# Optimization experiments

Measured on AMD Instinct MI355X. Metric: run time of the kernel, lower is better.

## Reference

```python
import jax, jax.numpy as jnp
import numpy as np

N, E = 50000, 800000
IN_DIM, HID, OUT = 64, 128, 64
EPS = 1e-5  # BatchNorm eps


def setup_inputs() -> dict:
    key = jax.random.key(0)
    ks = jax.random.split(key, 16)
    def w(k, i, o):
        return jax.random.normal(k, (i, o), jnp.float32) / np.float32(np.sqrt(i))
    def bn(k):
        km, kv = jax.random.split(k)
        return (jnp.ones((HID,), jnp.float32),                       # gamma
                jnp.zeros((HID,), jnp.float32),                      # beta
                0.1 * jax.random.normal(km, (HID,), jnp.float32),    # running mean
                0.5 + jax.random.uniform(kv, (HID,), jnp.float32))   # running var
    g0, be0, m0, v0 = bn(ks[6])
    g1, be1, m1, v1 = bn(ks[7])
    g2, be2, m2, v2 = bn(ks[8])
    return {
        "x":   jax.random.normal(ks[0], (N, IN_DIM), jnp.float32),
        "src": jax.random.randint(ks[1], (E,), 0, N, jnp.int32),
        "dst": jax.random.randint(ks[2], (E,), 0, N, jnp.int32),
        "W0": w(ks[3], IN_DIM, HID), "b0": jnp.zeros((HID,), jnp.float32),
        "g0": g0, "be0": be0, "m0": m0, "v0": v0,
        "W1": w(ks[4], HID, HID), "b1": jnp.zeros((HID,), jnp.float32),
        "g1": g1, "be1": be1, "m1": m1, "v1": v1,
        "W2": w(ks[5], HID, HID), "b2": jnp.zeros((HID,), jnp.float32),
        "g2": g2, "be2": be2, "m2": m2, "v2": v2,
        "Wm1": w(ks[9], HID, HID), "bm1": jnp.zeros((HID,), jnp.float32),
        "Wm2": w(ks[10], HID, OUT), "bm2": jnp.zeros((OUT,), jnp.float32),
    }


def gcn_conv(x, src, dst, W, b):
    # PyG GCNConv: h = x @ W; add self loops; symmetric normalization; scatter-add; + bias
    h = x @ W                                                     # [N, F]
    ones = jnp.ones((src.shape[0],), h.dtype)
    deg = 1.0 + jax.ops.segment_sum(ones, dst, num_segments=N)   # self loop adds 1
    dinv = jax.lax.rsqrt(deg)                                     # deg^-1/2 (deg >= 1)
    coef = (dinv[src] * dinv[dst])[:, None]                       # per-edge norm
    agg = jax.ops.segment_sum(h[src] * coef, dst, num_segments=N)
    return agg + h * (dinv * dinv)[:, None] + b                   # self-loop term + bias


def bn_relu(x, g, be, m, v):
    # eval-mode BatchNorm1d followed by ReLU (dropout is identity in eval)
    return jax.nn.relu((x - m) * jax.lax.rsqrt(v + EPS) * g + be)


def reference(x, src, dst,
              W0, b0, g0, be0, m0, v0,
              W1, b1, g1, be1, m1, v1,
              W2, b2, g2, be2, m2, v2,
              Wm1, bm1, Wm2, bm2):
    h = bn_relu(gcn_conv(x, src, dst, W0, b0), g0, be0, m0, v0)
    h = bn_relu(gcn_conv(h, src, dst, W1, b1), g1, be1, m1, v1)
    h = bn_relu(gcn_conv(h, src, dst, W2, b2), g2, be2, m2, v2)
    h = jax.nn.relu(h @ Wm1 + bm1)
    return h @ Wm2 + bm2
```

## Files before the change

### kernel.cpp

```cpp
#include <hip/hip_runtime.h>
#include <hip/hip_fp16.h>

#define BN_EPS 1e-5f
#define BK 512
#define NBMAX 128
#define ECH 8192
#define BCAP 9216

typedef _Float16 half_t;
typedef _Float16 half8 __attribute__((ext_vector_type(8)));
typedef float floatx4 __attribute__((ext_vector_type(4)));


__global__ __launch_bounds__(256) void scatter_cvt_kernel(
    const int* __restrict__ src, const int* __restrict__ dst,
    int* __restrict__ bcursor, int2* __restrict__ tmp,
    const float* __restrict__ x, __half* __restrict__ x16,
    int E, int nb, int sb, int n4) {
  const int t = threadIdx.x;
  if (blockIdx.x >= sb) {
    int i = (blockIdx.x - sb) * 256 + t;
    if (i < n4) {
      float4 v = *(const float4*)(x + (size_t)i * 4);
      union { __half h[4]; float2 f; } u;
      u.h[0] = __float2half_rn(v.x);
      u.h[1] = __float2half_rn(v.y);
      u.h[2] = __float2half_rn(v.z);
      u.h[3] = __float2half_rn(v.w);
      *(float2*)(x16 + (size_t)i * 4) = u.f;
    }
    return;
  }
  __shared__ int h[NBMAX];
  for (int i = t; i < nb; i += 256) h[i] = 0;
  __syncthreads();
  const int base = blockIdx.x * ECH;
#pragma unroll 8
  for (int p = 0; p < ECH / 256; ++p) {
    int e = base + p * 256 + t;
    if (e < E) atomicAdd(&h[dst[e] >> 9], 1);
  }
  __syncthreads();
  for (int i = t; i < nb; i += 256) {
    int c = h[i];
    h[i] = c ? (i * BCAP + atomicAdd(&bcursor[i], c)) : 0;
  }
  __syncthreads();
#pragma unroll 8
  for (int p = 0; p < ECH / 256; ++p) {
    int e = base + p * 256 + t;
    if (e < E) {
      int s = src[e], d = dst[e];
      int pos = atomicAdd(&h[d >> 9], 1);
      tmp[pos] = make_int2(s, d);
    }
  }
}

__global__ __launch_bounds__(256) void bucket_finalize_kernel(
    const int2* __restrict__ tmp, const int* __restrict__ bcursor,
    int* __restrict__ offs, int* __restrict__ offe, float* __restrict__ dinv,
    int* __restrict__ esrc, __half* __restrict__ x16, int n) {
  __shared__ int deg[BK];
  __shared__ int cur[BK];
  __shared__ float fdi[BK];
  __shared__ int ts[256];
  const int t = threadIdx.x;
  const int b = blockIdx.x;
  const int nbase = b * BK;
  const int nn = min(BK, n - nbase);
  const int cnt = bcursor[b];
  const int2* tp = tmp + (size_t)b * BCAP;
  for (int i = t; i < nn; i += 256) deg[i] = 0;
  __syncthreads();
  for (int e = t; e < cnt; e += 256)
    atomicAdd(&deg[tp[e].y - nbase], 1);
  __syncthreads();
  int d0 = (2 * t < nn) ? deg[2 * t] : 0;
  int d1 = (2 * t + 1 < nn) ? deg[2 * t + 1] : 0;
  ts[t] = d0 + d1;
  __syncthreads();
  for (int o = 1; o < 256; o <<= 1) {
    int v = (t >= o) ? ts[t - o] : 0;
    __syncthreads();
    ts[t] += v;
    __syncthreads();
  }
  int base = b * BCAP + ((t == 0) ? 0 : ts[t - 1]);
  if (2 * t < nn) {
    float di = rsqrtf(1.0f + (float)d0);
    offs[nbase + 2 * t] = base;
    offe[nbase + 2 * t] = base + d0;
    cur[2 * t] = base;
    fdi[2 * t] = di;
    dinv[nbase + 2 * t] = di;
  }
  if (2 * t + 1 < nn) {
    float di = rsqrtf(1.0f + (float)d1);
    offs[nbase + 2 * t + 1] = base + d0;
    offe[nbase + 2 * t + 1] = base + d0 + d1;
    cur[2 * t + 1] = base + d0;
    fdi[2 * t + 1] = di;
    dinv[nbase + 2 * t + 1] = di;
  }
  __syncthreads();
  for (int e = t; e < cnt; e += 256) {
    int2 r = tp[e];
    int pos = atomicAdd(&cur[r.y - nbase], 1);
    esrc[pos] = r.x;
  }
  __half2* xp = (__half2*)x16;
  for (int i = t; i < nn * 32; i += 256) {
    int nl = i >> 5;
    size_t idx = (((size_t)(nbase + nl)) << 5) + (i & 31);
    float2 v = __half22float2(xp[idx]);
    float s = fdi[nl];
    xp[idx] = __floats2half2_rn(v.x * s, v.y * s);
  }
}


template <int FIN, int FOUT, int EPI, bool HALFOUT>
__global__ __launch_bounds__(256) void mgemm_kernel(
    const __half* __restrict__ X, const float* __restrict__ W,
    const float* __restrict__ bias, const float* __restrict__ gam,
    const float* __restrict__ bet, const float* __restrict__ mean,
    const float* __restrict__ var, void* __restrict__ Yv, int n) {
  constexpr int LDK = 72;
  constexpr int NCI = FOUT / 16;
  __shared__ half_t Asm[128 * LDK];
  __shared__ half_t Bsm[FOUT * LDK];

  const int t = threadIdx.x;
  const int wave = t >> 6, lane = t & 63;
  const int quad = lane >> 4, l16 = lane & 15;
  const int rowBase = blockIdx.x * 128;

  floatx4 acc[2][NCI];
#pragma unroll
  for (int i = 0; i < 2; ++i)
#pragma unroll
    for (int ci = 0; ci < NCI; ++ci) acc[i][ci] = (floatx4){0.f, 0.f, 0.f, 0.f};

  for (int kc = 0; kc < FIN; kc += 64) {
    __syncthreads();
    {
      const int kq = t & 15, m0 = t >> 4;
#pragma unroll
      for (int p = 0; p < 8; ++p) {
        int m = p * 16 + m0;
        int row = rowBase + m;
        uint2 v = make_uint2(0u, 0u);
        if (row < n) v = *(const uint2*)(X + (size_t)row * FIN + kc + kq * 4);
        *(uint2*)&Asm[m * LDK + kq * 4] = v;
      }
    }
    {
#pragma unroll
      for (int c0 = 0; c0 < FOUT * 16; c0 += 256) {
        int c = c0 + t;
        int nn = c % FOUT;
        int kg = (c / FOUT) * 4;
        const float* wp = W + (size_t)(kc + kg) * FOUT + nn;
        half_t* d = &Bsm[nn * LDK + kg];
        d[0] = (half_t)wp[0];
        d[1] = (half_t)wp[FOUT];
        d[2] = (half_t)wp[2 * FOUT];
        d[3] = (half_t)wp[3 * FOUT];
      }
    }
    __syncthreads();
#pragma unroll
    for (int kk = 0; kk < 2; ++kk) {
      half8 a0 = *(const half8*)&Asm[(wave * 32 + l16) * LDK + kk * 32 + quad * 8];
      half8 a1 = *(const half8*)&Asm[(wave * 32 + 16 + l16) * LDK + kk * 32 + quad * 8];
#pragma unroll
      for (int ci = 0; ci < NCI; ++ci) {
        half8 b = *(const half8*)&Bsm[(ci * 16 + l16) * LDK + kk * 32 + quad * 8];
        acc[0][ci] = __builtin_amdgcn_mfma_f32_16x16x32_f16(a0, b, acc[0][ci], 0, 0, 0);
        acc[1][ci] = __builtin_amdgcn_mfma_f32_16x16x32_f16(a1, b, acc[1][ci], 0, 0, 0);
      }
    }
  }

  float sc[NCI], sh[NCI];
#pragma unroll
  for (int ci = 0; ci < NCI; ++ci) {
    int col = ci * 16 + l16;
    if constexpr (EPI == 3) {
      float s = gam[col] * rsqrtf(var[col] + BN_EPS);
      sc[ci] = s;
      sh[ci] = (bias[col] - mean[col]) * s + bet[col];
    } else if constexpr (EPI == 1 || EPI == 2) {
      sc[ci] = 1.f;
      sh[ci] = bias[col];
    } else {
      sc[ci] = 1.f;
      sh[ci] = 0.f;
    }
  }
  float rs[2][4];
  if constexpr (EPI == 4) {
#pragma unroll
    for (int ri = 0; ri < 2; ++ri)
#pragma unroll
      for (int r = 0; r < 4; ++r) {
        int row = rowBase + wave * 32 + ri * 16 + quad * 4 + r;
        rs[ri][r] = (row < n) ? bias[row] : 0.f;
      }
  }
#pragma unroll
  for (int ri = 0; ri < 2; ++ri)
#pragma unroll
    for (int ci = 0; ci < NCI; ++ci) {
      int col = ci * 16 + l16;
#pragma unroll
      for (int r = 0; r < 4; ++r) {
        int row = rowBase + wave * 32 + ri * 16 + quad * 4 + r;
        if (row < n) {
          float v = acc[ri][ci][r];
          if constexpr (EPI == 4) v *= rs[ri][r];
          if constexpr (EPI == 1 || EPI == 2 || EPI == 3) v = fmaf(v, sc[ci], sh[ci]);
          if constexpr (EPI == 1 || EPI == 3) v = fmaxf(v, 0.f);
          if constexpr (HALFOUT)
            ((half_t*)Yv)[(size_t)row * FOUT + col] = (half_t)v;
          else
            ((float*)Yv)[(size_t)row * FOUT + col] = v;
        }
      }
    }
}


__global__ __launch_bounds__(256) void mlp_kernel(
    const __half* __restrict__ X, const float* __restrict__ W1,
    const float* __restrict__ b1f, const float* __restrict__ W2,
    const float* __restrict__ b2f, float* __restrict__ Y, int n) {
  constexpr int LDK = 72;
  constexpr int LDK2 = 136;
  __shared__ half_t smem[(128 + 64) * LDK2];
  half_t* As1 = smem;
  half_t* Bs1 = smem + 128 * LDK;
  half_t* As2 = smem;
  half_t* Bs2 = smem + 128 * LDK2;

  const int t = threadIdx.x;
  const int wave = t >> 6, lane = t & 63;
  const int quad = lane >> 4, l16 = lane & 15;
  const int rowBase = blockIdx.x * 128;

  floatx4 acc[2][8];
#pragma unroll
  for (int i = 0; i < 2; ++i)
#pragma unroll
    for (int ci = 0; ci < 8; ++ci) acc[i][ci] = (floatx4){0.f, 0.f, 0.f, 0.f};

  for (int kc = 0; kc < 128; kc += 64) {
    __syncthreads();
    {
      const int kq = t & 15, m0 = t >> 4;
#pragma unroll
      for (int p = 0; p < 8; ++p) {
        int m = p * 16 + m0;
        int row = rowBase + m;
        uint2 v = make_uint2(0u, 0u);
        if (row < n) v = *(const uint2*)(X + (size_t)row * 128 + kc + kq * 4);
        *(uint2*)&As1[m * LDK + kq * 4] = v;
      }
    }
    {
#pragma unroll
      for (int c0 = 0; c0 < 128 * 16; c0 += 256) {
        int c = c0 + t;
        int nn = c & 127;
        int kg = (c >> 7) << 2;
        const float* wp = W1 + (size_t)(kc + kg) * 128 + nn;
        half_t* d = &Bs1[nn * LDK + kg];
        d[0] = (half_t)wp[0];
        d[1] = (half_t)wp[128];
        d[2] = (half_t)wp[256];
        d[3] = (half_t)wp[384];
      }
    }
    __syncthreads();
#pragma unroll
    for (int kk = 0; kk < 2; ++kk) {
      half8 a0 = *(const half8*)&As1[(wave * 32 + l16) * LDK + kk * 32 + quad * 8];
      half8 a1 = *(const half8*)&As1[(wave * 32 + 16 + l16) * LDK + kk * 32 + quad * 8];
#pragma unroll
      for (int ci = 0; ci < 8; ++ci) {
        half8 b = *(const half8*)&Bs1[(ci * 16 + l16) * LDK + kk * 32 + quad * 8];
        acc[0][ci] = __builtin_amdgcn_mfma_f32_16x16x32_f16(a0, b, acc[0][ci], 0, 0, 0);
        acc[1][ci] = __builtin_amdgcn_mfma_f32_16x16x32_f16(a1, b, acc[1][ci], 0, 0, 0);
      }
    }
  }
  __syncthreads();

#pragma unroll
  for (int ri = 0; ri < 2; ++ri)
#pragma unroll
    for (int ci = 0; ci < 8; ++ci) {
      int col = ci * 16 + l16;
      float bz = b1f[col];
#pragma unroll
      for (int r = 0; r < 4; ++r) {
        int m = wave * 32 + ri * 16 + quad * 4 + r;
        As2[m * LDK2 + col] = (half_t)fmaxf(acc[ri][ci][r] + bz, 0.f);
      }
    }
  {
#pragma unroll
    for (int c0 = 0; c0 < 64 * 32; c0 += 256) {
      int c = c0 + t;
      int nn = c & 63;
      int kg = (c >> 6) << 2;
      const float* wp = W2 + (size_t)kg * 64 + nn;
      half_t* d = &Bs2[nn * LDK2 + kg];
      d[0] = (half_t)wp[0];
      d[1] = (half_t)wp[64];
      d[2] = (half_t)wp[128];
      d[3] = (half_t)wp[192];
    }
  }
  __syncthreads();

  floatx4 acc2[2][4];
#pragma unroll
  for (int i = 0; i < 2; ++i)
#pragma unroll
    for (int ci = 0; ci < 4; ++ci) acc2[i][ci] = (floatx4){0.f, 0.f, 0.f, 0.f};
#pragma unroll
  for (int kk = 0; kk < 4; ++kk) {
    half8 a0 = *(const half8*)&As2[(wave * 32 + l16) * LDK2 + kk * 32 + quad * 8];
    half8 a1 = *(const half8*)&As2[(wave * 32 + 16 + l16) * LDK2 + kk * 32 + quad * 8];
#pragma unroll
    for (int ci = 0; ci < 4; ++ci) {
      half8 b = *(const half8*)&Bs2[(ci * 16 + l16) * LDK2 + kk * 32 + quad * 8];
      acc2[0][ci] = __builtin_amdgcn_mfma_f32_16x16x32_f16(a0, b, acc2[0][ci], 0, 0, 0);
      acc2[1][ci] = __builtin_amdgcn_mfma_f32_16x16x32_f16(a1, b, acc2[1][ci], 0, 0, 0);
    }
  }
#pragma unroll
  for (int ri = 0; ri < 2; ++ri)
#pragma unroll
    for (int ci = 0; ci < 4; ++ci) {
      int col = ci * 16 + l16;
      float bz = b2f[col];
#pragma unroll
      for (int r = 0; r < 4; ++r) {
        int row = rowBase + wave * 32 + ri * 16 + quad * 4 + r;
        if (row < n) Y[(size_t)row * 64 + col] = acc2[ri][ci][r] + bz;
      }
    }
}


__global__ __launch_bounds__(256) void agg64_kernel(
    const __half* __restrict__ h, const int* __restrict__ offs,
    const int* __restrict__ offe, const int* __restrict__ esrc,
    const float* __restrict__ dinv, __half* __restrict__ out, int n) {
  int gi = blockIdx.x * 4 + (threadIdx.x >> 6);
  if (gi >= n) return;
  const int lane = threadIdx.x & 63;
  const float di = dinv[gi];

  float a0 = 0.f, a1 = 0.f, a2 = 0.f, a3 = 0.f;
  int e = offs[gi];
  const int e1 = offe[gi];
  const int m = e1 - 1;
  for (; e < e1; e += 4) {
    int s0 = esrc[e];
    int s1 = esrc[min(e + 1, m)];
    int s2 = esrc[min(e + 2, m)];
    int s3 = esrc[min(e + 3, m)];
    float h0 = __half2float(h[((size_t)s0 << 6) + lane]);
    float h1 = __half2float(h[((size_t)s1 << 6) + lane]);
    float h2 = __half2float(h[((size_t)s2 << 6) + lane]);
    float h3 = __half2float(h[((size_t)s3 << 6) + lane]);
    if (e + 1 >= e1) h1 = 0.f;
    if (e + 2 >= e1) h2 = 0.f;
    if (e + 3 >= e1) h3 = 0.f;
    a0 += h0; a1 += h1; a2 += h2; a3 += h3;
  }
  float a = (a0 + a1) + (a2 + a3);
  a += __half2float(h[((size_t)gi << 6) + lane]);
  out[((size_t)gi << 6) + lane] = __float2half_rn(di * a);
}

__global__ __launch_bounds__(256) void agg128_bn_kernel(
    const __half* __restrict__ h, const int* __restrict__ offs,
    const int* __restrict__ offe, const int* __restrict__ esrc,
    const float* __restrict__ dinv,
    const float* __restrict__ bias, const float* __restrict__ gam,
    const float* __restrict__ bet, const float* __restrict__ mean,
    const float* __restrict__ var, __half* __restrict__ out, int n) {
  int gi = blockIdx.x * 4 + (threadIdx.x >> 6);
  if (gi >= n) return;
  const int lane = threadIdx.x & 63;
  const int c = lane << 1;
  const __half2* hp = (const __half2*)h;
  const float di = dinv[gi];

  float ax = 0.f, ay = 0.f, bx = 0.f, by = 0.f;
  float cx = 0.f, cy = 0.f, dx = 0.f, dy = 0.f;
  int e = offs[gi];
  const int e1 = offe[gi];
  const int m = e1 - 1;
  for (; e < e1; e += 4) {
    int s0 = esrc[e];
    int s1 = esrc[min(e + 1, m)];
    int s2 = esrc[min(e + 2, m)];
    int s3 = esrc[min(e + 3, m)];
    float2 h0 = __half22float2(hp[((size_t)s0 << 6) + lane]);
    float2 h1 = __half22float2(hp[((size_t)s1 << 6) + lane]);
    float2 h2 = __half22float2(hp[((size_t)s2 << 6) + lane]);
    float2 h3 = __half22float2(hp[((size_t)s3 << 6) + lane]);
    if (e + 1 >= e1) { h1.x = 0.f; h1.y = 0.f; }
    if (e + 2 >= e1) { h2.x = 0.f; h2.y = 0.f; }
    if (e + 3 >= e1) { h3.x = 0.f; h3.y = 0.f; }
    ax += h0.x; ay += h0.y; bx += h1.x; by += h1.y;
    cx += h2.x; cy += h2.y; dx += h3.x; dy += h3.y;
  }
  ax = (ax + bx) + (cx + dx);
  ay = (ay + by) + (cy + dy);
  float2 hs = __half22float2(hp[((size_t)gi << 6) + lane]);
  ax = di * (ax + hs.x);
  ay = di * (ay + hs.y);

  float2 bv = *(const float2*)(bias + c);
  float2 gv = *(const float2*)(gam + c);
  float2 bev = *(const float2*)(bet + c);
  float2 mv = *(const float2*)(mean + c);
  float2 vv = *(const float2*)(var + c);
  float s0 = gv.x * rsqrtf(vv.x + BN_EPS);
  float s1 = gv.y * rsqrtf(vv.y + BN_EPS);
  float o0 = fmaxf(fmaf(ax + bv.x - mv.x, s0, bev.x), 0.f);
  float o1 = fmaxf(fmaf(ay + bv.y - mv.y, s1, bev.y), 0.f);
  ((__half2*)out)[((size_t)gi << 6) + lane] = __floats2half2_rn(o0, o1);
}


static inline size_t alignup(size_t x, size_t a) { return (x + a - 1) & ~(a - 1); }

extern "C" void kernel_launch(void* const* d_in, const int* in_sizes, int n_in,
                              void* d_out, int out_size, void* d_ws, size_t ws_size,
                              hipStream_t stream) {
  const float* x   = (const float*)d_in[0];
  const int*   src = (const int*)d_in[1];
  const int*   dst = (const int*)d_in[2];
  const float* W0  = (const float*)d_in[3];
  const float* b0  = (const float*)d_in[4];
  const float* g0  = (const float*)d_in[5];
  const float* be0 = (const float*)d_in[6];
  const float* m0  = (const float*)d_in[7];
  const float* v0  = (const float*)d_in[8];
  const float* W1  = (const float*)d_in[9];
  const float* b1  = (const float*)d_in[10];
  const float* g1  = (const float*)d_in[11];
  const float* be1 = (const float*)d_in[12];
  const float* m1  = (const float*)d_in[13];
  const float* v1  = (const float*)d_in[14];
  const float* W2  = (const float*)d_in[15];
  const float* b2  = (const float*)d_in[16];
  const float* g2  = (const float*)d_in[17];
  const float* be2 = (const float*)d_in[18];
  const float* m2  = (const float*)d_in[19];
  const float* v2  = (const float*)d_in[20];
  const float* Wm1 = (const float*)d_in[21];
  const float* bm1 = (const float*)d_in[22];
  const float* Wm2 = (const float*)d_in[23];
  const float* bm2 = (const float*)d_in[24];

  const int N = in_sizes[0] / 64;
  const int E = in_sizes[1];

  char* p = (char*)d_ws;
  auto take = [&](size_t bytes) {
    char* r = p;
    p += alignup(bytes, 256);
    return r;
  };
  const int nbk = (N + BK - 1) / BK;
  int*    bcursor= (int*)take(NBMAX * 4);
  int*    offs   = (int*)take((size_t)N * 4);
  int*    offe   = (int*)take((size_t)N * 4);
  float*  dinv   = (float*)take((size_t)N * 4);
  int*    esrc   = (int*)take((size_t)nbk * BCAP * 4);
  int2*   tmp    = (int2*)take((size_t)nbk * BCAP * 8);
  __half* x16    = (__half*)take((size_t)N * 64 * 2);
  __half* aggx16 = (__half*)take((size_t)N * 64 * 2);
  __half* t0     = (__half*)take((size_t)N * 128 * 2);
  __half* t1     = (__half*)take((size_t)N * 128 * 2);
  float*  yout   = (float*)d_out;

  const int TB = 256;
  const int sb = (E + ECH - 1) / ECH;
  const int n4 = N * 16;
  const int cb = (n4 + 255) / 256;

  hipMemsetAsync(bcursor, 0, NBMAX * 4, stream);
  scatter_cvt_kernel<<<sb + cb, TB, 0, stream>>>(src, dst, bcursor, tmp,
                                                 x, x16, E, nbk, sb, n4);
  bucket_finalize_kernel<<<nbk, TB, 0, stream>>>(tmp, bcursor, offs, offe,
                                                 dinv, esrc, x16, N);

  const int gemmGrid = (N + 127) / 128;
  const int aggGrid = (N + 3) / 4;

  agg64_kernel<<<aggGrid, TB, 0, stream>>>(x16, offs, offe, esrc, dinv, aggx16, N);
  mgemm_kernel<64, 128, 3, true><<<gemmGrid, TB, 0, stream>>>(
      aggx16, W0, b0, g0, be0, m0, v0, t0, N);
  mgemm_kernel<128, 128, 4, true><<<gemmGrid, TB, 0, stream>>>(
      t0, W1, dinv, nullptr, nullptr, nullptr, nullptr, t1, N);
  agg128_bn_kernel<<<aggGrid, TB, 0, stream>>>(t1, offs, offe, esrc, dinv,
                                               b1, g1, be1, m1, v1, t0, N);
  mgemm_kernel<128, 128, 4, true><<<gemmGrid, TB, 0, stream>>>(
      t0, W2, dinv, nullptr, nullptr, nullptr, nullptr, t1, N);
  agg128_bn_kernel<<<aggGrid, TB, 0, stream>>>(t1, offs, offe, esrc, dinv,
                                               b2, g2, be2, m2, v2, t0, N);
  mlp_kernel<<<gemmGrid, TB, 0, stream>>>(t0, Wm1, bm1, Wm2, bm2, yout, N);
}
```

Baseline: 336.7 us.

## Split wave across edges with 8-byte row loads and shuffle reduction in aggregation

New measurement: 332.1 us. About the same (-1.4%).

```diff
diff --git a/kernel.cpp b/kernel.cpp
--- a/kernel.cpp
+++ b/kernel.cpp
@@ -363,29 +363,48 @@
   int gi = blockIdx.x * 4 + (threadIdx.x >> 6);
   if (gi >= n) return;
   const int lane = threadIdx.x & 63;
+  const int q = lane >> 4;
+  const int j = lane & 15;
+  const __half2* hp = (const __half2*)h;
   const float di = dinv[gi];
 
-  float a0 = 0.f, a1 = 0.f, a2 = 0.f, a3 = 0.f;
+  float ax = 0.f, ay = 0.f, az = 0.f, aw = 0.f;
+  float bx = 0.f, by = 0.f, bz = 0.f, bw = 0.f;
   int e = offs[gi];
   const int e1 = offe[gi];
   const int m = e1 - 1;
-  for (; e < e1; e += 4) {
-    int s0 = esrc[e];
-    int s1 = esrc[min(e + 1, m)];
-    int s2 = esrc[min(e + 2, m)];
-    int s3 = esrc[min(e + 3, m)];
-    float h0 = __half2float(h[((size_t)s0 << 6) + lane]);
-    float h1 = __half2float(h[((size_t)s1 << 6) + lane]);
-    float h2 = __half2float(h[((size_t)s2 << 6) + lane]);
-    float h3 = __half2float(h[((size_t)s3 << 6) + lane]);
-    if (e + 1 >= e1) h1 = 0.f;
-    if (e + 2 >= e1) h2 = 0.f;
-    if (e + 3 >= e1) h3 = 0.f;
-    a0 += h0; a1 += h1; a2 += h2; a3 += h3;
-  }
-  float a = (a0 + a1) + (a2 + a3);
-  a += __half2float(h[((size_t)gi << 6) + lane]);
-  out[((size_t)gi << 6) + lane] = __float2half_rn(di * a);
+  for (; e < e1; e += 8) {
+    int i0 = e + q;
+    int i1 = e + 4 + q;
+    int s0 = esrc[min(i0, m)];
+    int s1 = esrc[min(i1, m)];
+    uint2 r0 = *(const uint2*)(hp + (((size_t)s0) << 5) + j * 2);
+    uint2 r1 = *(const uint2*)(hp + (((size_t)s1) << 5) + j * 2);
+    if (i0 >= e1) { r0.x = 0u; r0.y = 0u; }
+    if (i1 >= e1) { r1.x = 0u; r1.y = 0u; }
+    float2 p0 = __half22float2(*(__half2*)&r0.x);
+    float2 p1 = __half22float2(*(__half2*)&r0.y);
+    float2 q0 = __half22float2(*(__half2*)&r1.x);
+    float2 q1 = __half22float2(*(__half2*)&r1.y);
+    ax += p0.x; ay += p0.y; az += p1.x; aw += p1.y;
+    bx += q0.x; by += q0.y; bz += q1.x; bw += q1.y;
+  }
+  ax += bx; ay += by; az += bz; aw += bw;
+  ax += __shfl_xor(ax, 16); ay += __shfl_xor(ay, 16);
+  az += __shfl_xor(az, 16); aw += __shfl_xor(aw, 16);
+  ax += __shfl_xor(ax, 32); ay += __shfl_xor(ay, 32);
+  az += __shfl_xor(az, 32); aw += __shfl_xor(aw, 32);
+  if (q == 0) {
+    uint2 rs = *(const uint2*)(hp + (((size_t)gi) << 5) + j * 2);
+    float2 s0 = __half22float2(*(__half2*)&rs.x);
+    float2 s1 = __half22float2(*(__half2*)&rs.y);
+    __half2 h0 = __floats2half2_rn(di * (ax + s0.x), di * (ay + s0.y));
+    __half2 h1 = __floats2half2_rn(di * (az + s1.x), di * (aw + s1.y));
+    uint2 ov;
+    ov.x = *(unsigned*)&h0;
+    ov.y = *(unsigned*)&h1;
+    *(uint2*)((__half2*)out + (((size_t)gi) << 5) + j * 2) = ov;
+  }
 }
 
 __global__ __launch_bounds__(256) void agg128_bn_kernel(
@@ -398,46 +417,60 @@
   int gi = blockIdx.x * 4 + (threadIdx.x >> 6);
   if (gi >= n) return;
   const int lane = threadIdx.x & 63;
-  const int c = lane << 1;
+  const int hh = lane >> 5;
+  const int j = lane & 31;
   const __half2* hp = (const __half2*)h;
   const float di = dinv[gi];
 
-  float ax = 0.f, ay = 0.f, bx = 0.f, by = 0.f;
-  float cx = 0.f, cy = 0.f, dx = 0.f, dy = 0.f;
+  float ax = 0.f, ay = 0.f, az = 0.f, aw = 0.f;
+  float bx = 0.f, by = 0.f, bz = 0.f, bw = 0.f;
   int e = offs[gi];
   const int e1 = offe[gi];
   const int m = e1 - 1;
   for (; e < e1; e += 4) {
-    int s0 = esrc[e];
-    int s1 = esrc[min(e + 1, m)];
-    int s2 = esrc[min(e + 2, m)];
-    int s3 = esrc[min(e + 3, m)];
-    float2 h0 = __half22float2(hp[((size_t)s0 << 6) + lane]);
-    float2 h1 = __half22float2(hp[((size_t)s1 << 6) + lane]);
-    float2 h2 = __half22float2(hp[((size_t)s2 << 6) + lane]);
-    float2 h3 = __half22float2(hp[((size_t)s3 << 6) + lane]);
-    if (e + 1 >= e1) { h1.x = 0.f; h1.y = 0.f; }
-    if (e + 2 >= e1) { h2.x = 0.f; h2.y = 0.f; }
-    if (e + 3 >= e1) { h3.x = 0.f; h3.y = 0.f; }
-    ax += h0.x; ay += h0.y; bx += h1.x; by += h1.y;
-    cx += h2.x; cy += h2.y; dx += h3.x; dy += h3.y;
-  }
-  ax = (ax + bx) + (cx + dx);
-  ay = (ay + by) + (cy + dy);
-  float2 hs = __half22float2(hp[((size_t)gi << 6) + lane]);
-  ax = di * (ax + hs.x);
-  ay = di * (ay + hs.y);
-
-  float2 bv = *(const float2*)(bias + c);
-  float2 gv = *(const float2*)(gam + c);
-  float2 bev = *(const float2*)(bet + c);
-  float2 mv = *(const float2*)(mean + c);
-  float2 vv = *(const float2*)(var + c);
-  float s0 = gv.x * rsqrtf(vv.x + BN_EPS);
-  float s1 = gv.y * rsqrtf(vv.y + BN_EPS);
-  float o0 = fmaxf(fmaf(ax + bv.x - mv.x, s0, bev.x), 0.f);
-  float o1 = fmaxf(fmaf(ay + bv.y - mv.y, s1, bev.y), 0.f);
-  ((__half2*)out)[((size_t)gi << 6) + lane] = __floats2half2_rn(o0, o1);
+    int i0 = e + hh;
+    int i1 = e + 2 + hh;
+    int s0 = esrc[min(i0, m)];
+    int s1 = esrc[min(i1, m)];
+    uint2 r0 = *(const uint2*)(hp + (((size_t)s0) << 6) + j * 2);
+    uint2 r1 = *(const uint2*)(hp + (((size_t)s1) << 6) + j * 2);
+    if (i0 >= e1) { r0.x = 0u; r0.y = 0u; }
+    if (i1 >= e1) { r1.x = 0u; r1.y = 0u; }
+    float2 p0 = __half22float2(*(__half2*)&r0.x);
+    float2 p1 = __half22float2(*(__half2*)&r0.y);
+    float2 q0 = __half22float2(*(__half2*)&r1.x);
+    float2 q1 = __half22float2(*(__half2*)&r1.y);
+    ax += p0.x; ay += p0.y; az += p1.x; aw += p1.y;
+    bx += q0.x; by += q0.y; bz += q1.x; bw += q1.y;
+  }
+  ax += bx; ay += by; az += bz; aw += bw;
+  ax += __shfl_xor(ax, 32); ay += __shfl_xor(ay, 32);
+  az += __shfl_xor(az, 32); aw += __shfl_xor(aw, 32);
+  if (hh == 0) {
+    uint2 rs = *(const uint2*)(hp + (((size_t)gi) << 6) + j * 2);
+    float2 s0 = __half22float2(*(__half2*)&rs.x);
+    float2 s1 = __half22float2(*(__half2*)&rs.y);
+    float v0 = di * (ax + s0.x);
+    float v1 = di * (ay + s0.y);
+    float v2 = di * (az + s1.x);
+    float v3 = di * (aw + s1.y);
+    const int c = j * 4;
+    float4 bv = *(const float4*)(bias + c);
+    float4 gv = *(const float4*)(gam + c);
+    float4 bev = *(const float4*)(bet + c);
+    float4 mv = *(const float4*)(mean + c);
+    float4 vv = *(const float4*)(var + c);
+    float o0 = fmaxf(fmaf(v0 + bv.x - mv.x, gv.x * rsqrtf(vv.x + BN_EPS), bev.x), 0.f);
+    float o1 = fmaxf(fmaf(v1 + bv.y - mv.y, gv.y * rsqrtf(vv.y + BN_EPS), bev.y), 0.f);
+    float o2 = fmaxf(fmaf(v2 + bv.z - mv.z, gv.z * rsqrtf(vv.z + BN_EPS), bev.z), 0.f);
+    float o3 = fmaxf(fmaf(v3 + bv.w - mv.w, gv.w * rsqrtf(vv.w + BN_EPS), bev.w), 0.f);
+    __half2 h0 = __floats2half2_rn(o0, o1);
+    __half2 h1 = __floats2half2_rn(o2, o3);
+    uint2 ov;
+    ov.x = *(unsigned*)&h0;
+    ov.y = *(unsigned*)&h1;
+    *(uint2*)((__half2*)out + (((size_t)gi) << 6) + j * 2) = ov;
+  }
 }
 
 
```

## Pack bucketed edges into 32-bit words and vectorize gather aggregation

Applied to the files above, without the earlier changes.

Result: faster. 323.3 us (-4.0%).

```diff
diff --git a/kernel.cpp b/kernel.cpp
--- a/kernel.cpp
+++ b/kernel.cpp
@@ -6,6 +6,7 @@
 #define NBMAX 128
 #define ECH 8192
 #define BCAP 9216
+#define ECAP 64
 
 typedef _Float16 half_t;
 typedef _Float16 half8 __attribute__((ext_vector_type(8)));
@@ -14,7 +15,7 @@
 
 __global__ __launch_bounds__(256) void scatter_cvt_kernel(
     const int* __restrict__ src, const int* __restrict__ dst,
-    int* __restrict__ bcursor, int2* __restrict__ tmp,
+    int* __restrict__ bcursor, unsigned* __restrict__ tmp,
     const float* __restrict__ x, __half* __restrict__ x16,
     int E, int nb, int sb, int n4) {
   const int t = threadIdx.x;
@@ -52,13 +53,13 @@
     if (e < E) {
       int s = src[e], d = dst[e];
       int pos = atomicAdd(&h[d >> 9], 1);
-      tmp[pos] = make_int2(s, d);
+      tmp[pos] = ((unsigned)s << 9) | (unsigned)(d & 511);
     }
   }
 }
 
 __global__ __launch_bounds__(256) void bucket_finalize_kernel(
-    const int2* __restrict__ tmp, const int* __restrict__ bcursor,
+    const unsigned* __restrict__ tmp, const int* __restrict__ bcursor,
     int* __restrict__ offs, int* __restrict__ offe, float* __restrict__ dinv,
     int* __restrict__ esrc, __half* __restrict__ x16, int n) {
   __shared__ int deg[BK];
@@ -70,11 +71,11 @@
   const int nbase = b * BK;
   const int nn = min(BK, n - nbase);
   const int cnt = bcursor[b];
-  const int2* tp = tmp + (size_t)b * BCAP;
+  const unsigned* tp = tmp + (size_t)b * BCAP;
   for (int i = t; i < nn; i += 256) deg[i] = 0;
   __syncthreads();
   for (int e = t; e < cnt; e += 256)
-    atomicAdd(&deg[tp[e].y - nbase], 1);
+    atomicAdd(&deg[tp[e] & 511u], 1);
   __syncthreads();
   int d0 = (2 * t < nn) ? deg[2 * t] : 0;
   int d1 = (2 * t + 1 < nn) ? deg[2 * t + 1] : 0;
@@ -105,9 +106,9 @@
   }
   __syncthreads();
   for (int e = t; e < cnt; e += 256) {
-    int2 r = tp[e];
-    int pos = atomicAdd(&cur[r.y - nbase], 1);
-    esrc[pos] = r.x;
+    unsigned r = tp[e];
+    int pos = atomicAdd(&cur[r & 511u], 1);
+    esrc[pos] = (int)(r >> 9);
   }
   __half2* xp = (__half2*)x16;
   for (int i = t; i < nn * 32; i += 256) {
@@ -356,36 +357,87 @@
 }
 
 
+__device__ __forceinline__ void acc8(uint4 r, float* a) {
+  float2 f;
+  f = __half22float2(*(__half2*)&r.x); a[0] += f.x; a[1] += f.y;
+  f = __half22float2(*(__half2*)&r.y); a[2] += f.x; a[3] += f.y;
+  f = __half22float2(*(__half2*)&r.z); a[4] += f.x; a[5] += f.y;
+  f = __half22float2(*(__half2*)&r.w); a[6] += f.x; a[7] += f.y;
+}
+
 __global__ __launch_bounds__(256) void agg64_kernel(
     const __half* __restrict__ h, const int* __restrict__ offs,
     const int* __restrict__ offe, const int* __restrict__ esrc,
     const float* __restrict__ dinv, __half* __restrict__ out, int n) {
-  int gi = blockIdx.x * 4 + (threadIdx.x >> 6);
+  __shared__ int eidx[4][ECAP];
+  const int wid = threadIdx.x >> 6;
+  int gi = blockIdx.x * 4 + wid;
   if (gi >= n) return;
   const int lane = threadIdx.x & 63;
+  const int slot = lane >> 3;
+  const int part = lane & 7;
+  const uint4* hp = (const uint4*)h;
   const float di = dinv[gi];
-
-  float a0 = 0.f, a1 = 0.f, a2 = 0.f, a3 = 0.f;
-  int e = offs[gi];
+  const int e0 = offs[gi];
   const int e1 = offe[gi];
-  const int m = e1 - 1;
-  for (; e < e1; e += 4) {
-    int s0 = esrc[e];
-    int s1 = esrc[min(e + 1, m)];
-    int s2 = esrc[min(e + 2, m)];
-    int s3 = esrc[min(e + 3, m)];
-    float h0 = __half2float(h[((size_t)s0 << 6) + lane]);
-    float h1 = __half2float(h[((size_t)s1 << 6) + lane]);
-    float h2 = __half2float(h[((size_t)s2 << 6) + lane]);
-    float h3 = __half2float(h[((size_t)s3 << 6) + lane]);
-    if (e + 1 >= e1) h1 = 0.f;
-    if (e + 2 >= e1) h2 = 0.f;
-    if (e + 3 >= e1) h3 = 0.f;
-    a0 += h0; a1 += h1; a2 += h2; a3 += h3;
-  }
-  float a = (a0 + a1) + (a2 + a3);
-  a += __half2float(h[((size_t)gi << 6) + lane]);
-  out[((size_t)gi << 6) + lane] = __float2half_rn(di * a);
+  const int deg = e1 - e0;
+  const int dm = min(deg, ECAP);
+  if (lane < dm) eidx[wid][lane] = esrc[e0 + lane];
+
+  float a[8] = {0.f, 0.f, 0.f, 0.f, 0.f, 0.f, 0.f, 0.f};
+  float b[8] = {0.f, 0.f, 0.f, 0.f, 0.f, 0.f, 0.f, 0.f};
+  int k = 0;
+  for (; k + 16 <= dm; k += 16) {
+    int s0 = eidx[wid][k + slot];
+    int s1 = eidx[wid][k + 8 + slot];
+    uint4 r0 = hp[(((size_t)s0) << 3) + part];
+    uint4 r1 = hp[(((size_t)s1) << 3) + part];
+    acc8(r0, a);
+    acc8(r1, b);
+  }
+  const int mm = dm - 1;
+  const uint4 z = make_uint4(0u, 0u, 0u, 0u);
+  for (; k < dm; k += 16) {
+    int i0 = k + slot, i1 = k + 8 + slot;
+    int s0 = eidx[wid][min(i0, mm)];
+    int s1 = eidx[wid][min(i1, mm)];
+    uint4 r0 = hp[(((size_t)s0) << 3) + part];
+    uint4 r1 = hp[(((size_t)s1) << 3) + part];
+    if (i0 >= dm) r0 = z;
+    if (i1 >= dm) r1 = z;
+    acc8(r0, a);
+    acc8(r1, b);
+  }
+  for (int e = e0 + ECAP; e < e1; e += 8) {
+    int i0 = e + slot;
+    int s0 = esrc[min(i0, e1 - 1)];
+    uint4 r0 = hp[(((size_t)s0) << 3) + part];
+    if (i0 >= e1) r0 = z;
+    acc8(r0, a);
+  }
+#pragma unroll
+  for (int i = 0; i < 8; ++i) a[i] += b[i];
+#pragma unroll
+  for (int i = 0; i < 8; ++i) {
+    a[i] += __shfl_xor(a[i], 8);
+    a[i] += __shfl_xor(a[i], 16);
+    a[i] += __shfl_xor(a[i], 32);
+  }
+  if (slot == 0) {
+    uint4 rs = hp[(((size_t)gi) << 3) + part];
+    float s[8] = {0.f, 0.f, 0.f, 0.f, 0.f, 0.f, 0.f, 0.f};
+    acc8(rs, s);
+    __half2 h0 = __floats2half2_rn(di * (a[0] + s[0]), di * (a[1] + s[1]));
+    __half2 h1 = __floats2half2_rn(di * (a[2] + s[2]), di * (a[3] + s[3]));
+    __half2 h2 = __floats2half2_rn(di * (a[4] + s[4]), di * (a[5] + s[5]));
+    __half2 h3 = __floats2half2_rn(di * (a[6] + s[6]), di * (a[7] + s[7]));
+    uint4 ov;
+    ov.x = *(unsigned*)&h0;
+    ov.y = *(unsigned*)&h1;
+    ov.z = *(unsigned*)&h2;
+    ov.w = *(unsigned*)&h3;
+    ((uint4*)out)[(((size_t)gi) << 3) + part] = ov;
+  }
 }
 
 __global__ __launch_bounds__(256) void agg128_bn_kernel(
@@ -395,49 +447,98 @@
     const float* __restrict__ bias, const float* __restrict__ gam,
     const float* __restrict__ bet, const float* __restrict__ mean,
     const float* __restrict__ var, __half* __restrict__ out, int n) {
-  int gi = blockIdx.x * 4 + (threadIdx.x >> 6);
+  __shared__ int eidx[4][ECAP];
+  const int wid = threadIdx.x >> 6;
+  int gi = blockIdx.x * 4 + wid;
   if (gi >= n) return;
   const int lane = threadIdx.x & 63;
-  const int c = lane << 1;
-  const __half2* hp = (const __half2*)h;
+  const int slot = lane >> 4;
+  const int part = lane & 15;
+  const uint4* hp = (const uint4*)h;
   const float di = dinv[gi];
-
-  float ax = 0.f, ay = 0.f, bx = 0.f, by = 0.f;
-  float cx = 0.f, cy = 0.f, dx = 0.f, dy = 0.f;
-  int e = offs[gi];
+  const int e0 = offs[gi];
   const int e1 = offe[gi];
-  const int m = e1 - 1;
-  for (; e < e1; e += 4) {
-    int s0 = esrc[e];
-    int s1 = esrc[min(e + 1, m)];
-    int s2 = esrc[min(e + 2, m)];
-    int s3 = esrc[min(e + 3, m)];
-    float2 h0 = __half22float2(hp[((size_t)s0 << 6) + lane]);
-    float2 h1 = __half22float2(hp[((size_t)s1 << 6) + lane]);
-    float2 h2 = __half22float2(hp[((size_t)s2 << 6) + lane]);
-    float2 h3 = __half22float2(hp[((size_t)s3 << 6) + lane]);
-    if (e + 1 >= e1) { h1.x = 0.f; h1.y = 0.f; }
-    if (e + 2 >= e1) { h2.x = 0.f; h2.y = 0.f; }
-    if (e + 3 >= e1) { h3.x = 0.f; h3.y = 0.f; }
-    ax += h0.x; ay += h0.y; bx += h1.x; by += h1.y;
-    cx += h2.x; cy += h2.y; dx += h3.x; dy += h3.y;
-  }
-  ax = (ax + bx) + (cx + dx);
-  ay = (ay + by) + (cy + dy);
-  float2 hs = __half22float2(hp[((size_t)gi << 6) + lane]);
-  ax = di * (ax + hs.x);
-  ay = di * (ay + hs.y);
-
-  float2 bv = *(const float2*)(bias + c);
-  float2 gv = *(const float2*)(gam + c);
-  float2 bev = *(const float2*)(bet + c);
-  float2 mv = *(const float2*)(mean + c);
-  float2 vv = *(const float2*)(var + c);
-  float s0 = gv.x * rsqrtf(vv.x + BN_EPS);
-  float s1 = gv.y * rsqrtf(vv.y + BN_EPS);
-  float o0 = fmaxf(fmaf(ax + bv.x - mv.x, s0, bev.x), 0.f);
-  float o1 = fmaxf(fmaf(ay + bv.y - mv.y, s1, bev.y), 0.f);
-  ((__half2*)out)[((size_t)gi << 6) + lane] = __floats2half2_rn(o0, o1);
+  const int deg = e1 - e0;
+  const int dm = min(deg, ECAP);
+  if (lane < dm) eidx[wid][lane] = esrc[e0 + lane];
+
+  float a[8] = {0.f, 0.f, 0.f, 0.f, 0.f, 0.f, 0.f, 0.f};
+  float b[8] = {0.f, 0.f, 0.f, 0.f, 0.f, 0.f, 0.f, 0.f};
+  int k = 0;
+  for (; k + 16 <= dm; k += 16) {
+    int s0 = eidx[wid][k + slot];
+    int s1 = eidx[wid][k + 4 + slot];
+    int s2 = eidx[wid][k + 8 + slot];
+    int s3 = eidx[wid][k + 12 + slot];
+    uint4 r0 = hp[(((size_t)s0) << 4) + part];
+    uint4 r1 = hp[(((size_t)s1) << 4) + part];
+    uint4 r2 = hp[(((size_t)s2) << 4) + part];
+    uint4 r3 = hp[(((size_t)s3) << 4) + part];
+    acc8(r0, a);
+    acc8(r1, b);
+    acc8(r2, a);
+    acc8(r3, b);
+  }
+  const int mm = dm - 1;
+  const uint4 z = make_uint4(0u, 0u, 0u, 0u);
+  for (; k < dm; k += 8) {
+    int i0 = k + slot, i1 = k + 4 + slot;
+    int s0 = eidx[wid][min(i0, mm)];
+    int s1 = eidx[wid][min(i1, mm)];
+    uint4 r0 = hp[(((size_t)s0) << 4) + part];
+    uint4 r1 = hp[(((size_t)s1) << 4) + part];
+    if (i0 >= dm) r0 = z;
+    if (i1 >= dm) r1 = z;
+    acc8(r0, a);
+    acc8(r1, b);
+  }
+  for (int e = e0 + ECAP; e < e1; e += 4) {
+    int i0 = e + slot;
+    int s0 = esrc[min(i0, e1 - 1)];
+    uint4 r0 = hp[(((size_t)s0) << 4) + part];
+    if (i0 >= e1) r0 = z;
+    acc8(r0, a);
+  }
+#pragma unroll
+  for (int i = 0; i < 8; ++i) a[i] += b[i];
+#pragma unroll
+  for (int i = 0; i < 8; ++i) {
+    a[i] += __shfl_xor(a[i], 16);
+    a[i] += __shfl_xor(a[i], 32);
+  }
+  if (slot == 0) {
+    uint4 rs = hp[(((size_t)gi) << 4) + part];
+    float s[8] = {0.f, 0.f, 0.f, 0.f, 0.f, 0.f, 0.f, 0.f};
+    acc8(rs, s);
+    const int c = part * 8;
+    float o[8];
+#pragma unroll
+    for (int i = 0; i < 8; i += 4) {
+      float4 bv = *(const float4*)(bias + c + i);
+      float4 gv = *(const float4*)(gam + c + i);
+      float4 bev = *(const float4*)(bet + c + i);
+      float4 mv = *(const float4*)(mean + c + i);
+      float4 vv = *(const float4*)(var + c + i);
+      float v0 = di * (a[i + 0] + s[i + 0]);
+      float v1 = di * (a[i + 1] + s[i + 1]);
+      float v2 = di * (a[i + 2] + s[i + 2]);
+      float v3 = di * (a[i + 3] + s[i + 3]);
+      o[i + 0] = fmaxf(fmaf(v0 + bv.x - mv.x, gv.x * rsqrtf(vv.x + BN_EPS), bev.x), 0.f);
+      o[i + 1] = fmaxf(fmaf(v1 + bv.y - mv.y, gv.y * rsqrtf(vv.y + BN_EPS), bev.y), 0.f);
+      o[i + 2] = fmaxf(fmaf(v2 + bv.z - mv.z, gv.z * rsqrtf(vv.z + BN_EPS), bev.z), 0.f);
+      o[i + 3] = fmaxf(fmaf(v3 + bv.w - mv.w, gv.w * rsqrtf(vv.w + BN_EPS), bev.w), 0.f);
+    }
+    __half2 h0 = __floats2half2_rn(o[0], o[1]);
+    __half2 h1 = __floats2half2_rn(o[2], o[3]);
+    __half2 h2 = __floats2half2_rn(o[4], o[5]);
+    __half2 h3 = __floats2half2_rn(o[6], o[7]);
+    uint4 ov;
+    ov.x = *(unsigned*)&h0;
+    ov.y = *(unsigned*)&h1;
+    ov.z = *(unsigned*)&h2;
+    ov.w = *(unsigned*)&h3;
+    ((uint4*)out)[(((size_t)gi) << 4) + part] = ov;
+  }
 }
 
 
@@ -482,17 +583,17 @@
     return r;
   };
   const int nbk = (N + BK - 1) / BK;
-  int*    bcursor= (int*)take(NBMAX * 4);
-  int*    offs   = (int*)take((size_t)N * 4);
-  int*    offe   = (int*)take((size_t)N * 4);
-  float*  dinv   = (float*)take((size_t)N * 4);
-  int*    esrc   = (int*)take((size_t)nbk * BCAP * 4);
-  int2*   tmp    = (int2*)take((size_t)nbk * BCAP * 8);
-  __half* x16    = (__half*)take((size_t)N * 64 * 2);
-  __half* aggx16 = (__half*)take((size_t)N * 64 * 2);
-  __half* t0     = (__half*)take((size_t)N * 128 * 2);
-  __half* t1     = (__half*)take((size_t)N * 128 * 2);
-  float*  yout   = (float*)d_out;
+  int*      bcursor= (int*)take(NBMAX * 4);
+  int*      offs   = (int*)take((size_t)N * 4);
+  int*      offe   = (int*)take((size_t)N * 4);
+  float*    dinv   = (float*)take((size_t)N * 4);
+  int*      esrc   = (int*)take((size_t)nbk * BCAP * 4);
+  unsigned* tmp    = (unsigned*)take((size_t)nbk * BCAP * 4);
+  __half*   x16    = (__half*)take((size_t)N * 64 * 2);
+  __half*   aggx16 = (__half*)take((size_t)N * 64 * 2);
+  __half*   t0     = (__half*)take((size_t)N * 128 * 2);
+  __half*   t1     = (__half*)take((size_t)N * 128 * 2);
+  float*    yout   = (float*)d_out;
 
   const int TB = 256;
   const int sb = (E + ECH - 1) / ECH;
```
